# Kernel tuning notes

Measured on AMD Instinct MI355X. Metric: run time of the kernel, lower is better.

Reference implementation:

```python
import jax, jax.numpy as jnp
import numpy as np


def _mw_weight(m):
    if m == 1:
        return 1j * np.pi / 2
    if m == -1:
        return -1j * np.pi / 2
    if m % 2 == 0:
        return 2.0 / (1 - m * m)
    return 0.0


def quad_weights_mw(L):
    # Exact MW quadrature weights (McEwen & Wiaux 2011), folded to L theta samples.
    ms = np.arange(-(L - 1), L)
    w = np.array([_mw_weight(m) for m in ms], dtype=np.complex128)
    w *= np.exp(-1j * ms * np.pi / (2 * L - 1))
    wr = np.real(np.fft.fft(np.fft.ifftshift(w))) / (2 * L - 1)
    q = wr[:L].copy()
    q[: L - 1] += wr[2 * L - 2 : L - 1 : -1]  # fold extended-grid weights (spin=0)
    return q * 2 * np.pi / (2 * L - 1)


def legendre_table(L, theta):
    # Normalized assoc. Legendre Pbar_{lm}(cos theta) incl. sqrt((2l+1)/4pi (l-m)!/(l+m)!)
    # and Condon-Shortley phase. Returns (L, 2L-1, ntheta) with m index = m + L - 1.
    ct, st = np.cos(theta), np.sin(theta)
    nt = theta.shape[0]
    P = np.zeros((L, L, nt))
    P[0, 0] = 1.0 / np.sqrt(4 * np.pi)
    for m in range(1, L):
        P[m, m] = -np.sqrt((2 * m + 1) / (2.0 * m)) * st * P[m - 1, m - 1]
    for m in range(0, L - 1):
        P[m + 1, m] = np.sqrt(2 * m + 3.0) * ct * P[m, m]
    for m in range(0, L):
        for l in range(m + 2, L):
            a = np.sqrt((4.0 * l * l - 1) / (l * l - m * m))
            b = np.sqrt(((2.0 * l + 1) * ((l - 1) ** 2 - m * m)) / ((2.0 * l - 3) * (l * l - m * m)))
            P[l, m] = a * ct * P[l - 1, m] - b * P[l - 2, m]
    full = np.zeros((L, 2 * L - 1, nt))
    for m in range(0, L):
        full[:, L - 1 + m] = P[:, m]
        if m > 0:
            full[:, L - 1 - m] = ((-1) ** m) * P[:, m]
    return full


def _mw_theta(L):
    return np.pi * (2 * np.arange(L) + 1) / (2 * L - 1)


def sht_forward(f, L, plm, weights):
    # f: (L, 2L-1, C) real -> flm: (L, 2L-1, C) complex
    nphi = 2 * L - 1
    ms = np.arange(-(L - 1), L)
    Fm = jnp.fft.fft(f, axis=1)[:, ms % nphi, :]  # (ntheta, 2L-1, C)
    return jnp.einsum('t,lmt,tmc->lmc', weights, plm, Fm)


def sht_inverse(flm, L, plm):
    # flm: (L, 2L-1, C) complex -> real field (L, 2L-1, C)
    nphi = 2 * L - 1
    ms = np.arange(-(L - 1), L)
    G = jnp.einsum('lmc,lmt->tmc', flm, plm)  # (ntheta, 2L-1, C)
    Gfull = jnp.zeros_like(G).at[:, ms % nphi, :].set(G)
    return jnp.real(jnp.fft.ifft(Gfull, axis=1) * nphi)


def resize_flm(flm, L_new):
    L_old = flm.shape[0]
    if L_new == L_old:
        return flm
    if L_new < L_old:
        return flm[:L_new, L_old - L_new : L_old + L_new - 1]
    out = jnp.zeros((L_new, 2 * L_new - 1) + flm.shape[2:], flm.dtype)
    return out.at[:L_old, L_new - L_old : L_new + L_old - 1].set(flm)


def setup_inputs() -> dict:
    key = jax.random.key(0)
    ks = jax.random.split(key, 6)
    L_in, Lf, L_out = 128, 64, 128
    Cin, Cout, T = 64, 64, 256
    return {
        'x': jax.random.normal(ks[0], (L_in, 2 * L_in - 1, Cin), jnp.float32),
        't_emb': jax.random.normal(ks[1], (T,), jnp.float32),
        'A_real': 0.01 * jax.random.normal(ks[2], (Lf, 2 * Lf - 1, T), jnp.float32),
        'A_imag': 0.01 * jax.random.normal(ks[3], (Lf, 2 * Lf - 1, T), jnp.float32),
        'R_real': 0.01 * jax.random.normal(ks[4], (Lf, 2 * Lf - 1, Cout, Cin), jnp.float32),
        'R_imag': 0.01 * jax.random.normal(ks[5], (Lf, 2 * Lf - 1, Cout, Cin), jnp.float32),
        'L_out_spatial': L_out,
    }


def reference(x, t_emb, A_real, A_imag, R_real, R_imag, L_out_spatial):
    L_in = x.shape[0]
    Lf = A_real.shape[0]
    plm_in = jnp.asarray(legendre_table(L_in, _mw_theta(L_in)), jnp.float32)
    w_in = jnp.asarray(quad_weights_mw(L_in), jnp.float32)
    flm = sht_forward(x, L_in, plm_in, w_in)            # (L_in, 2L_in-1, Cin)
    flm = resize_flm(flm, Lf)                           # (Lf, 2Lf-1, Cin)
    t_c = (jnp.einsum('t,lmt->lm', t_emb, A_real)
           + 1j * jnp.einsum('t,lmt->lm', t_emb, A_imag))
    R = R_real + 1j * R_imag                            # (Lf, 2Lf-1, O, I)
    Rt = jnp.einsum('lm,lmoi->loi', t_c, R)
    flm_out = jnp.einsum('lmi,loi->lmo', flm, Rt)
    flm_out = resize_flm(flm_out, L_out_spatial)
    plm_out = jnp.asarray(legendre_table(L_out_spatial, _mw_theta(L_out_spatial)), jnp.float32)
    return sht_inverse(flm_out, L_out_spatial, plm_out)  # (L_out, 2L_out-1, O)
```

## Files before the change

kernel.cpp:

```cpp
#include <hip/hip_runtime.h>
#include <math.h>

#define PI_D 3.14159265358979323846
static const size_t OFF_P   = 0;
static const size_t OFF_W   = 524288;
static const size_t OFF_TW  = 524416;
static const size_t OFF_FMW = 524928;
static const size_t OFF_TC  = 1573504;
static const size_t OFF_FLM = 1589760;
static const size_t OFF_RT  = 2114048;
static const size_t OFF_FO  = 2638336;
static const size_t OFF_G   = 524928;
static const size_t WS_FLOATS = 3678720;

__global__ __launch_bounds__(256) void k_tables(float* __restrict__ w, float2* __restrict__ tw) {
  int t = blockIdx.x;
  int tid = threadIdx.x;
  if (t == 0 && tid < 255) {
    double a = 2.0 * PI_D * tid / 255.0;
    tw[tid] = make_float2((float)cos(a), (float)sin(a));
  }
  double term = 0.0;
  if (tid < 255) {
    int m = tid - 127;
    double br = 0.0, bi = 0.0; bool active = true;
    if (m == 1) bi = PI_D / 2.0;
    else if (m == -1) bi = -PI_D / 2.0;
    else if ((m & 1) == 0) br = 2.0 / (1.0 - (double)m * (double)m);
    else active = false;
    if (active) {
      double md = (double)m;
      double ca = cos(PI_D * md / 255.0), sa = -sin(PI_D * md / 255.0);
      double wr = br * ca - bi * sa;
      double wi = br * sa + bi * ca;
      double a1 = 2.0 * PI_D * md * t / 255.0;
      double fr = cos(a1), fi = -sin(a1);
      if (t < 127) {
        double a2 = 2.0 * PI_D * md * (t + 1) / 255.0;
        fr += cos(a2); fi += sin(a2);
      }
      term = wr * fr - wi * fi;
    }
  }
  __shared__ double red[256];
  red[tid] = term;
  __syncthreads();
  for (int off = 128; off; off >>= 1) {
    if (tid < off) red[tid] += red[tid + off];
    __syncthreads();
  }
  if (tid == 0) w[t] = (float)(red[0] * 2.0 * PI_D / (255.0 * 255.0));
}

__global__ __launch_bounds__(128) void k_legendre(float* __restrict__ P) {
  int m = blockIdx.x, t = threadIdx.x;
  double th = PI_D * (2 * t + 1) / 255.0;
  double ct = cos(th), st = sin(th);
  double pmm = 0.28209479177387814;
  for (int k = 1; k <= m; ++k) pmm *= -sqrt((2.0 * k + 1.0) / (2.0 * k)) * st;
  float* Pm = P + ((size_t)m * 64) * 128;
  Pm[(size_t)m * 128 + t] = (float)pmm;
  if (m + 1 < 64) {
    double p0 = pmm, p1 = sqrt(2.0 * m + 3.0) * ct * pmm;
    Pm[(size_t)(m + 1) * 128 + t] = (float)p1;
    for (int l = m + 2; l < 64; ++l) {
      double ll = (double)l * l, mm = (double)m * m;
      double a = sqrt((4.0 * ll - 1.0) / (ll - mm));
      double b = sqrt((2.0 * l + 1.0) * ((double)(l - 1) * (l - 1) - mm) / ((2.0 * l - 3.0) * (ll - mm)));
      double pl = a * ct * p1 - b * p0;
      Pm[(size_t)l * 128 + t] = (float)pl;
      p0 = p1; p1 = pl;
    }
  }
}

__global__ __launch_bounds__(256) void k_fwd_dft(const float* __restrict__ x, const float* __restrict__ w,
                                                 const float2* __restrict__ tw, float2* __restrict__ Fmw) {
  int t = blockIdx.x, mq = blockIdx.y;
  __shared__ float xs[255 * 64];
  int tid = threadIdx.x;
  for (int idx = tid; idx < 255 * 64; idx += 256) xs[idx] = x[(size_t)t * (255 * 64) + idx];
  __syncthreads();
  int c = tid & 63, ms = tid >> 6;
  int m0 = mq * 8 + ms * 2;
  float2 wm0 = tw[m0], wm1 = tw[m0 + 1];
  float cr0 = wm0.x, ci0 = -wm0.y;
  float cr1 = wm1.x, ci1 = -wm1.y;
  float tr0 = 1.f, ti0 = 0.f, tr1 = 1.f, ti1 = 0.f;
  float a0r = 0.f, a0i = 0.f, a1r = 0.f, a1i = 0.f;
#pragma unroll 5
  for (int p = 0; p < 255; ++p) {
    float xv = xs[p * 64 + c];
    a0r += xv * tr0; a0i += xv * ti0;
    a1r += xv * tr1; a1i += xv * ti1;
    float n0 = tr0 * cr0 - ti0 * ci0; ti0 = tr0 * ci0 + ti0 * cr0; tr0 = n0;
    float n1 = tr1 * cr1 - ti1 * ci1; ti1 = tr1 * ci1 + ti1 * cr1; tr1 = n1;
  }
  float wt = w[t];
  Fmw[((size_t)m0 * 128 + t) * 64 + c] = make_float2(wt * a0r, wt * a0i);
  Fmw[((size_t)(m0 + 1) * 128 + t) * 64 + c] = make_float2(wt * a1r, wt * a1i);
}

__global__ __launch_bounds__(256) void k_tc(const float* __restrict__ te, const float* __restrict__ Ar,
                                            const float* __restrict__ Ai, float2* __restrict__ tc) {
  int bid = blockIdx.x;
  int tid = threadIdx.x;
  float e = te[tid];
  float vr = Ar[(size_t)bid * 256 + tid] * e;
  float vi = Ai[(size_t)bid * 256 + tid] * e;
  for (int off = 32; off; off >>= 1) {
    vr += __shfl_down(vr, off);
    vi += __shfl_down(vi, off);
  }
  __shared__ float2 red[4];
  if ((tid & 63) == 0) red[tid >> 6] = make_float2(vr, vi);
  __syncthreads();
  if (tid == 0) {
    float2 s = red[0];
    for (int q = 1; q < 4; ++q) { s.x += red[q].x; s.y += red[q].y; }
    tc[bid] = s;
  }
}

__global__ __launch_bounds__(256) void k_rt(const float* __restrict__ Rr, const float* __restrict__ Ri,
                                            const float2* __restrict__ tc, float2* __restrict__ Rt) {
  int l = blockIdx.x, og = blockIdx.y;
  int tid = threadIdx.x;
  __shared__ float2 tcs[127];
  if (tid < 127) tcs[tid] = tc[l * 127 + tid];
  __syncthreads();
  int ic = tid & 15, ol = tid >> 4;
  int o = og * 16 + ol;
  const float* rr = Rr + ((size_t)l * 127) * 4096 + o * 64 + ic * 4;
  const float* ri = Ri + ((size_t)l * 127) * 4096 + o * 64 + ic * 4;
  float4 ar = make_float4(0.f, 0.f, 0.f, 0.f);
  float4 ai = make_float4(0.f, 0.f, 0.f, 0.f);
#pragma unroll 4
  for (int j = 0; j < 127; ++j) {
    float2 w2 = tcs[j];
    float4 a = *reinterpret_cast<const float4*>(rr + (size_t)j * 4096);
    float4 b = *reinterpret_cast<const float4*>(ri + (size_t)j * 4096);
    ar.x += w2.x * a.x - w2.y * b.x;  ai.x += w2.x * b.x + w2.y * a.x;
    ar.y += w2.x * a.y - w2.y * b.y;  ai.y += w2.x * b.y + w2.y * a.y;
    ar.z += w2.x * a.z - w2.y * b.z;  ai.z += w2.x * b.z + w2.y * a.z;
    ar.w += w2.x * a.w - w2.y * b.w;  ai.w += w2.x * b.w + w2.y * a.w;
  }
  float4* rt4 = reinterpret_cast<float4*>(Rt);
  size_t base = ((size_t)l * 64 + o) * 32 + ic * 2;
  rt4[base]     = make_float4(ar.x, ai.x, ar.y, ai.y);
  rt4[base + 1] = make_float4(ar.z, ai.z, ar.w, ai.w);
}

__global__ __launch_bounds__(256) void k_flm(const float* __restrict__ P, const float2* __restrict__ Fmw,
                                             float2* __restrict__ flm) {
  int m = blockIdx.x, lq = blockIdx.y;
  int tid = threadIdx.x;
  int c = tid & 63, lg = tid >> 6;
  __shared__ float2 Fs[32][64];
  __shared__ float Ps[8][32];
  float2 acc[2];
  acc[0] = make_float2(0.f, 0.f);
  acc[1] = make_float2(0.f, 0.f);
  for (int q = 0; q < 4; ++q) {
    __syncthreads();
    for (int idx = tid; idx < 2048; idx += 256) {
      int tt = idx >> 6, cc = idx & 63;
      Fs[tt][cc] = Fmw[((size_t)m * 128 + q * 32 + tt) * 64 + cc];
    }
    {
      int ll = tid >> 5, tt2 = tid & 31;
      int l = m + lq * 8 + ll;
      Ps[ll][tt2] = (l < 64) ? P[((size_t)m * 64 + l) * 128 + q * 32 + tt2] : 0.f;
    }
    __syncthreads();
    int li = lg * 2;
#pragma unroll 8
    for (int tt = 0; tt < 32; ++tt) {
      float2 f = Fs[tt][c];
      float p0 = Ps[li][tt], p1 = Ps[li + 1][tt];
      acc[0].x += p0 * f.x; acc[0].y += p0 * f.y;
      acc[1].x += p1 * f.x; acc[1].y += p1 * f.y;
    }
  }
#pragma unroll
  for (int s = 0; s < 2; ++s) {
    int l = m + lq * 8 + lg * 2 + s;
    if (l < 64) flm[((size_t)l * 64 + m) * 64 + c] = acc[s];
  }
}

__global__ __launch_bounds__(256) void k_flmout(const float2* __restrict__ flm, const float2* __restrict__ Rt,
                                                float2* __restrict__ fo) {
  int l = blockIdx.x, jg = blockIdx.y;
  int o = threadIdx.x & 63, js = threadIdx.x >> 6;
  __shared__ float2 Rts[64][65];
  __shared__ float2 Fjs[16][64];
  for (int idx = threadIdx.x; idx < 4096; idx += 256) {
    int oo = idx >> 6, ii = idx & 63;
    Rts[oo][ii] = Rt[((size_t)l * 64 + oo) * 64 + ii];
  }
  for (int idx = threadIdx.x; idx < 1024; idx += 256) {
    int jl = idx >> 6, ii = idx & 63;
    int j = jg * 16 + jl;
    float2 v = make_float2(0.f, 0.f);
    if (j < 127) {
      int mm = j - 63, am = mm < 0 ? -mm : mm;
      if (l >= am) {
        float2 f = flm[((size_t)l * 64 + am) * 64 + ii];
        if (mm < 0) { float s = (am & 1) ? -1.f : 1.f; v = make_float2(s * f.x, -s * f.y); }
        else v = f;
      }
    }
    Fjs[jl][ii] = v;
  }
  __syncthreads();
  float2 acc[4];
#pragma unroll
  for (int q = 0; q < 4; ++q) acc[q] = make_float2(0.f, 0.f);
  for (int i = 0; i < 64; ++i) {
    float2 r = Rts[o][i];
#pragma unroll
    for (int q = 0; q < 4; ++q) {
      float2 f = Fjs[js * 4 + q][i];
      acc[q].x += f.x * r.x - f.y * r.y;
      acc[q].y += f.x * r.y + f.y * r.x;
    }
  }
#pragma unroll
  for (int q = 0; q < 4; ++q) {
    int j = jg * 16 + js * 4 + q;
    if (j < 127) fo[((size_t)l * 127 + j) * 64 + o] = acc[q];
  }
}

__global__ __launch_bounds__(256) void k_g(const float* __restrict__ P, const float2* __restrict__ fo,
                                           float2* __restrict__ G) {
  int j = blockIdx.x, tg = blockIdx.y;
  int mm = j - 63, am = mm < 0 ? -mm : mm;
  float sgn = (mm < 0 && (am & 1)) ? -1.f : 1.f;
  int o = threadIdx.x & 63, ts = threadIdx.x >> 6;
  __shared__ float Ps[64][64];
  __shared__ float2 Fos[64][64];
  for (int idx = threadIdx.x; idx < 4096; idx += 256) {
    int ll = idx >> 6, tt = idx & 63;
    Ps[ll][tt] = P[((size_t)am * 64 + ll) * 128 + tg * 64 + tt];
  }
  for (int idx = threadIdx.x; idx < 4096; idx += 256) {
    int ll = idx >> 6, oo = idx & 63;
    float2 v = fo[((size_t)ll * 127 + j) * 64 + oo];
    Fos[ll][oo] = make_float2(sgn * v.x, sgn * v.y);
  }
  __syncthreads();
  float ar[16], ai2[16];
#pragma unroll
  for (int r = 0; r < 16; ++r) { ar[r] = 0.f; ai2[r] = 0.f; }
  for (int l = am; l < 64; ++l) {
    float2 f = Fos[l][o];
#pragma unroll
    for (int q = 0; q < 4; ++q) {
      float4 pv = *reinterpret_cast<const float4*>(&Ps[l][ts * 16 + q * 4]);
      ar[q * 4 + 0] += pv.x * f.x;  ai2[q * 4 + 0] += pv.x * f.y;
      ar[q * 4 + 1] += pv.y * f.x;  ai2[q * 4 + 1] += pv.y * f.y;
      ar[q * 4 + 2] += pv.z * f.x;  ai2[q * 4 + 2] += pv.z * f.y;
      ar[q * 4 + 3] += pv.w * f.x;  ai2[q * 4 + 3] += pv.w * f.y;
    }
  }
#pragma unroll
  for (int r = 0; r < 16; ++r) {
    int t = tg * 64 + ts * 16 + r;
    G[((size_t)t * 127 + j) * 64 + o] = make_float2(ar[r], ai2[r]);
  }
}

__global__ __launch_bounds__(256) void k_idft(const float2* __restrict__ G, const float2* __restrict__ tw,
                                              float* __restrict__ out) {
  int t = blockIdx.x, pq = blockIdx.y;
  int pl = threadIdx.x & 63, og = threadIdx.x >> 6;
  __shared__ __align__(16) unsigned char smem[65536];
  float2 (*CSs)[64] = reinterpret_cast<float2(*)[64]>(smem);
  float (*Ls)[65] = reinterpret_cast<float(*)[65]>(smem);
  for (int idx = threadIdx.x; idx < 4096; idx += 256) {
    int m = idx >> 6, oo = idx & 63;
    float2 v;
    if (m == 0) {
      float2 g = G[((size_t)t * 127 + 63) * 64 + oo];
      v = make_float2(g.x, 0.f);
    } else {
      float2 gp = G[((size_t)t * 127 + 63 + m) * 64 + oo];
      float2 gm = G[((size_t)t * 127 + 63 - m) * 64 + oo];
      v = make_float2(gp.x + gm.x, gm.y - gp.y);
    }
    CSs[m][oo] = v;
  }
  __syncthreads();
  int p = pq * 64 + pl;
  float2 wp = tw[p < 255 ? p : 0];
  float twr = 1.f, twi = 0.f;
  float acc[16];
#pragma unroll
  for (int r = 0; r < 16; ++r) acc[r] = 0.f;
  int ob = og * 16;
  for (int m = 0; m < 64; ++m) {
#pragma unroll
    for (int q = 0; q < 8; ++q) {
      float4 cs = *reinterpret_cast<const float4*>(&CSs[m][ob + q * 2]);
      acc[q * 2 + 0] += cs.x * twr + cs.y * twi;
      acc[q * 2 + 1] += cs.z * twr + cs.w * twi;
    }
    float nr = twr * wp.x - twi * wp.y;
    twi = twr * wp.y + twi * wp.x;
    twr = nr;
  }
  __syncthreads();
#pragma unroll
  for (int r = 0; r < 16; ++r) Ls[pl][ob + r] = acc[r];
  __syncthreads();
  for (int idx = threadIdx.x; idx < 4096; idx += 256) {
    int rr = idx >> 6, oo = idx & 63;
    int pg = pq * 64 + rr;
    if (pg < 255) out[((size_t)t * 255 + pg) * 64 + oo] = Ls[rr][oo];
  }
}

extern "C" void kernel_launch(void* const* d_in, const int* in_sizes, int n_in,
                              void* d_out, int out_size, void* d_ws, size_t ws_size,
                              hipStream_t stream) {
  (void)in_sizes; (void)n_in; (void)out_size;
  if (ws_size < WS_FLOATS * sizeof(float)) return;

  const float* x  = (const float*)d_in[0];
  const float* te = (const float*)d_in[1];
  const float* Ar = (const float*)d_in[2];
  const float* Ai = (const float*)d_in[3];
  const float* Rr = (const float*)d_in[4];
  const float* Ri = (const float*)d_in[5];
  float* out = (float*)d_out;

  float* ws = (float*)d_ws;
  float*  P   = ws + OFF_P;
  float*  w   = ws + OFF_W;
  float2* tw  = (float2*)(ws + OFF_TW);
  float2* Fmw = (float2*)(ws + OFF_FMW);
  float2* tc  = (float2*)(ws + OFF_TC);
  float2* flm = (float2*)(ws + OFF_FLM);
  float2* Rt  = (float2*)(ws + OFF_RT);
  float2* fo  = (float2*)(ws + OFF_FO);
  float2* G   = (float2*)(ws + OFF_G);

  k_tables<<<128, 256, 0, stream>>>(w, tw);
  k_legendre<<<64, 128, 0, stream>>>(P);
  k_fwd_dft<<<dim3(128, 8), 256, 0, stream>>>(x, w, tw, Fmw);
  k_tc<<<64 * 127, 256, 0, stream>>>(te, Ar, Ai, tc);
  k_rt<<<dim3(64, 4), 256, 0, stream>>>(Rr, Ri, tc, Rt);
  k_flm<<<dim3(64, 8), 256, 0, stream>>>(P, Fmw, flm);
  k_flmout<<<dim3(64, 8), 256, 0, stream>>>(flm, Rt, fo);
  k_g<<<dim3(127, 2), 256, 0, stream>>>(P, fo, G);
  k_idft<<<dim3(128, 4), 256, 0, stream>>>(G, tw, out);
}
```

Before: 429.2 us.

## Split Rt contraction over m into partial sums with separate reduction kernel

The Rt kernel now splits the 127-element m reduction into four chunks across blockIdx.y, so each block reads a contiguous slab of R per m with fully coalesced float4 loads. Each chunk writes partial sums into scratch buffers (reusing Fmw and fo workspace regions), and a new small kernel adds the four partials. k_rt is moved after k_flm so the Fmw region is free to hold partials. The change trades an extra launch and extra global traffic for better memory access patterns in the bandwidth-heavy R read.

Measured after the change: 432.3 us. No clear change (+0.7%).

```diff
diff --git a/kernel.cpp b/kernel.cpp
--- a/kernel.cpp
+++ b/kernel.cpp
@@ -11,6 +11,9 @@
 static const size_t OFF_RT  = 2114048;
 static const size_t OFF_FO  = 2638336;
 static const size_t OFF_G   = 524928;
+static const size_t OFF_P1  = OFF_FO;
+static const size_t OFF_P2  = OFF_FMW;
+static const size_t OFF_P3  = OFF_FMW + 524288;
 static const size_t WS_FLOATS = 3678720;
 
 __global__ __launch_bounds__(256) void k_tables(float* __restrict__ w, float2* __restrict__ tw) {
@@ -123,32 +126,70 @@
 }
 
 __global__ __launch_bounds__(256) void k_rt(const float* __restrict__ Rr, const float* __restrict__ Ri,
-                                            const float2* __restrict__ tc, float2* __restrict__ Rt) {
-  int l = blockIdx.x, og = blockIdx.y;
+                                            const float2* __restrict__ tc,
+                                            float2* __restrict__ pp0, float2* __restrict__ pp1,
+                                            float2* __restrict__ pp2, float2* __restrict__ pp3) {
+  int l = blockIdx.x, jq = blockIdx.y;
   int tid = threadIdx.x;
   __shared__ float2 tcs[127];
   if (tid < 127) tcs[tid] = tc[l * 127 + tid];
   __syncthreads();
-  int ic = tid & 15, ol = tid >> 4;
-  int o = og * 16 + ol;
-  const float* rr = Rr + ((size_t)l * 127) * 4096 + o * 64 + ic * 4;
-  const float* ri = Ri + ((size_t)l * 127) * 4096 + o * 64 + ic * 4;
-  float4 ar = make_float4(0.f, 0.f, 0.f, 0.f);
-  float4 ai = make_float4(0.f, 0.f, 0.f, 0.f);
-#pragma unroll 4
-  for (int j = 0; j < 127; ++j) {
+  int j0 = jq * 32, j1 = (jq == 3) ? 127 : (j0 + 32);
+  const float* rr = Rr + ((size_t)l * 127 + j0) * 4096 + tid * 4;
+  const float* ri = Ri + ((size_t)l * 127 + j0) * 4096 + tid * 4;
+  float4 ar0 = make_float4(0.f,0.f,0.f,0.f), ai0 = ar0;
+  float4 ar1 = ar0, ai1 = ar0, ar2 = ar0, ai2 = ar0, ar3 = ar0, ai3 = ar0;
+#pragma unroll 2
+  for (int j = j0; j < j1; ++j) {
     float2 w2 = tcs[j];
-    float4 a = *reinterpret_cast<const float4*>(rr + (size_t)j * 4096);
-    float4 b = *reinterpret_cast<const float4*>(ri + (size_t)j * 4096);
-    ar.x += w2.x * a.x - w2.y * b.x;  ai.x += w2.x * b.x + w2.y * a.x;
-    ar.y += w2.x * a.y - w2.y * b.y;  ai.y += w2.x * b.y + w2.y * a.y;
-    ar.z += w2.x * a.z - w2.y * b.z;  ai.z += w2.x * b.z + w2.y * a.z;
-    ar.w += w2.x * a.w - w2.y * b.w;  ai.w += w2.x * b.w + w2.y * a.w;
-  }
-  float4* rt4 = reinterpret_cast<float4*>(Rt);
-  size_t base = ((size_t)l * 64 + o) * 32 + ic * 2;
-  rt4[base]     = make_float4(ar.x, ai.x, ar.y, ai.y);
-  rt4[base + 1] = make_float4(ar.z, ai.z, ar.w, ai.w);
+    float4 a0 = *reinterpret_cast<const float4*>(rr);
+    float4 a1 = *reinterpret_cast<const float4*>(rr + 1024);
+    float4 a2 = *reinterpret_cast<const float4*>(rr + 2048);
+    float4 a3 = *reinterpret_cast<const float4*>(rr + 3072);
+    float4 b0 = *reinterpret_cast<const float4*>(ri);
+    float4 b1 = *reinterpret_cast<const float4*>(ri + 1024);
+    float4 b2 = *reinterpret_cast<const float4*>(ri + 2048);
+    float4 b3 = *reinterpret_cast<const float4*>(ri + 3072);
+    ar0.x += w2.x*a0.x - w2.y*b0.x;  ai0.x += w2.x*b0.x + w2.y*a0.x;
+    ar0.y += w2.x*a0.y - w2.y*b0.y;  ai0.y += w2.x*b0.y + w2.y*a0.y;
+    ar0.z += w2.x*a0.z - w2.y*b0.z;  ai0.z += w2.x*b0.z + w2.y*a0.z;
+    ar0.w += w2.x*a0.w - w2.y*b0.w;  ai0.w += w2.x*b0.w + w2.y*a0.w;
+    ar1.x += w2.x*a1.x - w2.y*b1.x;  ai1.x += w2.x*b1.x + w2.y*a1.x;
+    ar1.y += w2.x*a1.y - w2.y*b1.y;  ai1.y += w2.x*b1.y + w2.y*a1.y;
+    ar1.z += w2.x*a1.z - w2.y*b1.z;  ai1.z += w2.x*b1.z + w2.y*a1.z;
+    ar1.w += w2.x*a1.w - w2.y*b1.w;  ai1.w += w2.x*b1.w + w2.y*a1.w;
+    ar2.x += w2.x*a2.x - w2.y*b2.x;  ai2.x += w2.x*b2.x + w2.y*a2.x;
+    ar2.y += w2.x*a2.y - w2.y*b2.y;  ai2.y += w2.x*b2.y + w2.y*a2.y;
+    ar2.z += w2.x*a2.z - w2.y*b2.z;  ai2.z += w2.x*b2.z + w2.y*a2.z;
+    ar2.w += w2.x*a2.w - w2.y*b2.w;  ai2.w += w2.x*b2.w + w2.y*a2.w;
+    ar3.x += w2.x*a3.x - w2.y*b3.x;  ai3.x += w2.x*b3.x + w2.y*a3.x;
+    ar3.y += w2.x*a3.y - w2.y*b3.y;  ai3.y += w2.x*b3.y + w2.y*a3.y;
+    ar3.z += w2.x*a3.z - w2.y*b3.z;  ai3.z += w2.x*b3.z + w2.y*a3.z;
+    ar3.w += w2.x*a3.w - w2.y*b3.w;  ai3.w += w2.x*b3.w + w2.y*a3.w;
+    rr += 4096; ri += 4096;
+  }
+  float2* outp = (jq == 0) ? pp0 : (jq == 1) ? pp1 : (jq == 2) ? pp2 : pp3;
+  float4* out4 = reinterpret_cast<float4*>(outp);
+  int ic = tid & 15, orow = tid >> 4;
+#define RT_STORE(Q, AR, AI)                                              \
+  {                                                                      \
+    size_t base = ((size_t)l * 64 + (Q) * 16 + orow) * 32 + ic * 2;      \
+    out4[base]     = make_float4(AR.x, AI.x, AR.y, AI.y);                \
+    out4[base + 1] = make_float4(AR.z, AI.z, AR.w, AI.w);                \
+  }
+  RT_STORE(0, ar0, ai0)
+  RT_STORE(1, ar1, ai1)
+  RT_STORE(2, ar2, ai2)
+  RT_STORE(3, ar3, ai3)
+#undef RT_STORE
+}
+
+__global__ __launch_bounds__(256) void k_rtred(float4* __restrict__ pp0, const float4* __restrict__ pp1,
+                                               const float4* __restrict__ pp2, const float4* __restrict__ pp3) {
+  int idx = blockIdx.x * 256 + threadIdx.x;
+  float4 a = pp0[idx], b = pp1[idx], c = pp2[idx], d = pp3[idx];
+  pp0[idx] = make_float4(a.x + b.x + c.x + d.x, a.y + b.y + c.y + d.y,
+                         a.z + b.z + c.z + d.z, a.w + b.w + c.w + d.w);
 }
 
 __global__ __launch_bounds__(256) void k_flm(const float* __restrict__ P, const float2* __restrict__ Fmw,
@@ -346,13 +387,17 @@
   float2* Rt  = (float2*)(ws + OFF_RT);
   float2* fo  = (float2*)(ws + OFF_FO);
   float2* G   = (float2*)(ws + OFF_G);
+  float2* p1  = (float2*)(ws + OFF_P1);
+  float2* p2  = (float2*)(ws + OFF_P2);
+  float2* p3  = (float2*)(ws + OFF_P3);
 
   k_tables<<<128, 256, 0, stream>>>(w, tw);
   k_legendre<<<64, 128, 0, stream>>>(P);
   k_fwd_dft<<<dim3(128, 8), 256, 0, stream>>>(x, w, tw, Fmw);
   k_tc<<<64 * 127, 256, 0, stream>>>(te, Ar, Ai, tc);
-  k_rt<<<dim3(64, 4), 256, 0, stream>>>(Rr, Ri, tc, Rt);
   k_flm<<<dim3(64, 8), 256, 0, stream>>>(P, Fmw, flm);
+  k_rt<<<dim3(64, 4), 256, 0, stream>>>(Rr, Ri, tc, Rt, p1, p2, p3);
+  k_rtred<<<512, 256, 0, stream>>>((float4*)Rt, (const float4*)p1, (const float4*)p2, (const float4*)p3);
   k_flmout<<<dim3(64, 8), 256, 0, stream>>>(flm, Rt, fo);
   k_g<<<dim3(127, 2), 256, 0, stream>>>(P, fo, G);
   k_idft<<<dim3(128, 4), 256, 0, stream>>>(G, tw, out);
```
